# Optimization experiments

Hardware: AMD Instinct MI355X
Metric: run time of the kernel (lower is better)

The kernel has to match this reference:

```python
import jax, jax.numpy as jnp
import numpy as np
from jax import lax

B, C, HW = 128, 32, 16
N_E = 4096
PNS = (1, 2, 3, 4, 5, 6, 8, 10, 13, 16)
SN = len(PNS)
BETA, RESI = 0.25, 0.5
EPS = 1e-12

# PhiPartiallyShared tick schedule (K=4): which of the 4 Phi convs each scale uses
_TICKS = np.linspace(1.0 / 12.0, 1.0 - 1.0 / 12.0, 4)
PHI_IDX = [int(np.argmin(np.abs(_TICKS - si / (SN - 1)))) for si in range(SN)]


def _cubic_w(t, a=-0.75):
    # PyTorch bicubic kernel (a = -0.75)
    t = np.abs(t)
    return np.where(t <= 1.0, ((a + 2.0) * t - (a + 3.0)) * t * t + 1.0,
                    np.where(t < 2.0, (((t - 5.0) * t + 8.0) * t - 4.0) * a, 0.0))


def _bicubic_mat(n_in, n_out):
    # 1D resize matrix matching F.interpolate(mode='bicubic', align_corners=False)
    M = np.zeros((n_out, n_in), np.float32)
    scale = n_in / n_out
    for i in range(n_out):
        src = (i + 0.5) * scale - 0.5
        i0 = int(np.floor(src))
        f = src - i0
        for off in (-1, 0, 1, 2):
            w = float(_cubic_w(f - off))
            j = min(max(i0 + off, 0), n_in - 1)  # border replicate
            M[i, j] += w
    return M


def _area_mat(n_in, n_out):
    # 1D matrix matching F.interpolate(mode='area') == adaptive_avg_pool
    M = np.zeros((n_out, n_in), np.float32)
    for i in range(n_out):
        s = (i * n_in) // n_out
        e = -(-((i + 1) * n_in) // n_out)  # ceil
        M[i, s:e] = 1.0 / (e - s)
    return M


DOWN = {pn: jnp.asarray(_area_mat(HW, pn)) for pn in PNS[:-1]}
UP = {pn: jnp.asarray(_bicubic_mat(pn, HW)) for pn in PNS[:-1]}


def _resize2(x, M):
    # separable 2D resize: x [B,C,Y,X] -> [B,C,O,P]
    return jnp.einsum('oy,px,bcyx->bcop', M, M, x)


def _phi(h, w, b):
    conv = lax.conv_general_dilated(h, w, (1, 1), ((1, 1), (1, 1)),
                                    dimension_numbers=('NCHW', 'OIHW', 'NCHW'))
    conv = conv + b[None, :, None, None]
    return h * (1.0 - RESI) + conv * RESI


def _forward(f_input, codebook, phi_w, phi_b):
    f_ng = lax.stop_gradient(f_input)
    f_rest = f_ng
    f_hat = jnp.zeros_like(f_ng)
    cb_n = codebook / jnp.maximum(jnp.linalg.norm(codebook, axis=-1, keepdims=True), EPS)
    loss = jnp.asarray(0.0, jnp.float32)
    idx = None
    for si, pn in enumerate(PNS):
        x = _resize2(f_rest, DOWN[pn]) if si != SN - 1 else f_rest
        rest = x.transpose(0, 2, 3, 1).reshape(-1, C)          # [B*pn*pn, C]
        rest_n = rest / jnp.maximum(jnp.linalg.norm(rest, axis=-1, keepdims=True), EPS)
        idx = jnp.argmax(rest_n @ cb_n.T, axis=1)              # cosine-sim argmax
        h = codebook[idx].reshape(B, pn, pn, C).transpose(0, 3, 1, 2)
        if si != SN - 1:
            h = _resize2(h, UP[pn])
        k = PHI_IDX[si]
        h = _phi(h, phi_w[k], phi_b[k])
        f_hat = f_hat + h
        f_rest = f_rest - h
        loss = loss + BETA * jnp.mean((lax.stop_gradient(f_hat) - f_input) ** 2) \
                    + jnp.mean((f_hat - f_ng) ** 2)
    loss = loss / SN
    # straight-through estimator
    f_hat_st = f_input + lax.stop_gradient(f_hat - f_input)
    return f_hat_st, loss, idx


def setup_inputs() -> dict:
    key = jax.random.key(0)
    k1, k2, k3, k4 = jax.random.split(key, 4)
    return {
        'f_input': jax.random.normal(k1, (B, C, HW, HW), jnp.float32),
        'codebook': jax.random.normal(k2, (N_E, C), jnp.float32) * 0.5,
        'phi_w': jax.random.normal(k3, (4, C, C, 3, 3), jnp.float32) * (1.0 / np.sqrt(C * 9)),
        'phi_b': jax.random.normal(k4, (4, C), jnp.float32) * 0.01,
    }


def reference(f_input, codebook, phi_w, phi_b):
    f_hat, loss, idx = _forward(f_input, codebook, phi_w, phi_b)
    # perplexity of last-scale code usage
    n_tok = idx.shape[0]
    avg_probs = jnp.zeros((N_E,), jnp.float32).at[idx].add(1.0) / n_tok
    perplexity = jnp.exp(-jnp.sum(avg_probs * jnp.log(avg_probs + 1e-10)))
    return f_hat, loss, perplexity
```

## Files before the change

kernel.cpp:

```cpp
#include <hip/hip_runtime.h>
#include <stdint.h>
#include <math.h>


#define DEVI __device__ __forceinline__

static constexpr int NE = 4096;

typedef _Float16 half8 __attribute__((ext_vector_type(8)));
typedef float floatx4 __attribute__((ext_vector_type(4)));

DEVI int imax(int a, int b) { return a > b ? a : b; }

DEVI float dppL(float v) {
    return __int_as_float(
        __builtin_amdgcn_update_dpp(0, __float_as_int(v), 0x111, 0xF, 0xF, true));
}
DEVI float dppR(float v) {
    return __int_as_float(
        __builtin_amdgcn_update_dpp(0, __float_as_int(v), 0x101, 0xF, 0xF, true));
}

__global__ void __launch_bounds__(256) k_setup(const float* __restrict__ cb,
                                               const float* __restrict__ pw,
                                               _Float16* __restrict__ cbh,
                                               _Float16* __restrict__ cbl,
                                               float* __restrict__ wT,
                                               float* __restrict__ um,
                                               float* __restrict__ lossAcc) {
    int blk = blockIdx.x, tid = threadIdx.x;
    if (blk < 16) {
        int r = blk * 256 + tid;
        const float* src = cb + r * 32;
        float v[32];
        float ss = 0.f;
#pragma unroll
        for (int j = 0; j < 32; ++j) { v[j] = src[j]; ss += v[j] * v[j]; }
        float n = fmaxf(sqrtf(ss), 1e-12f);
#pragma unroll
        for (int j = 0; j < 32; ++j) {
            float x = v[j] / n;
            _Float16 h = (_Float16)x;
            cbh[r * 32 + j] = h;
            cbl[r * 32 + j] = (_Float16)(x - (float)h);
        }
    } else if (blk < 160) {
        int e = (blk - 16) * 256 + tid;
        int k = e / 9216, rem = e % 9216;
        int q8 = rem / 1152, rem2 = rem % 1152;
        int ic = rem2 / 36, r3 = rem2 % 36;
        int k9 = r3 / 4, o2 = r3 % 4;
        int oc = (q8 >> 2) * 16 + (q8 & 3) * 4 + o2;
        int ky = k9 / 3, kx = k9 % 3;
        wT[e] = pw[(((k * 32 + oc) * 32 + ic) * 3 + ky) * 3 + kx];
    } else {
        if (tid < 144) {
            const int pns[9] = {1, 2, 3, 4, 5, 6, 8, 10, 13};
            int si = tid / 16, y = tid % 16, pn = pns[si];
            double scale = (double)pn / 16.0;
            double src = ((double)y + 0.5) * scale - 0.5;
            double fl = floor(src);
            int i0 = (int)fl;
            double f = src - fl;
            float row[13];
            for (int j = 0; j < pn; ++j) row[j] = 0.f;
            const double a = -0.75;
#pragma unroll
            for (int off = -1; off <= 2; ++off) {
                double t2 = fabs(f - (double)off);
                double wgt;
                if (t2 <= 1.0)      wgt = ((a + 2.0) * t2 - (a + 3.0)) * t2 * t2 + 1.0;
                else if (t2 < 2.0)  wgt = (((t2 - 5.0) * t2 + 8.0) * t2 - 4.0) * a;
                else                wgt = 0.0;
                int j = i0 + off;
                j = j < 0 ? 0 : (j > pn - 1 ? pn - 1 : j);
                row[j] = (float)((double)row[j] + wgt);
            }
            for (int j = 0; j < pn; ++j) um[si * 256 + y * pn + j] = row[j];
        } else {
            for (int i = tid - 144; i < 4112; i += 112) ((int*)lossAcc)[i] = 0;
        }
    }
}


template <int PN, bool FIRST>
__global__ void __launch_bounds__(256) k_down(const float* __restrict__ fin,
                                              const float* __restrict__ fhat,
                                              _Float16* __restrict__ xh,
                                              _Float16* __restrict__ xl) {
    constexpr int NT = PN * PN;
    constexpr int T = 128 * NT;
    constexpr int Tp = ((T + 511) / 512) * 512;
    int tid = threadIdx.x;
    if (blockIdx.x >= 256) {
        for (int i = tid; i < (Tp - T) * 32; i += 256) {
            xh[T * 32 + i] = (_Float16)0.f;
            xl[T * 32 + i] = (_Float16)0.f;
        }
        return;
    }
    __shared__ float r[16][260];
    int img = blockIdx.x >> 1, ch = (blockIdx.x & 1) * 16;

    const float4* pi4 = (const float4*)(fin + img * 8192 + ch * 256);
    const float4* ph4 = (const float4*)(fhat + img * 8192 + ch * 256);
    for (int i = tid; i < 1024; i += 256) {
        float4 a = pi4[i];
        float4 b;
        if constexpr (FIRST) { b.x = 0.f; b.y = 0.f; b.z = 0.f; b.w = 0.f; }
        else                 { b = ph4[i]; }
        int c = i >> 6, p = (i & 63) * 4;
        r[c][p]     = a.x - b.x;
        r[c][p + 1] = a.y - b.y;
        r[c][p + 2] = a.z - b.z;
        r[c][p + 3] = a.w - b.w;
    }
    __syncthreads();

    for (int e = tid; e < NT * 16; e += 256) {
        int lt = e >> 4, cp = e & 15;
        int oy = lt / PN, ox = lt % PN;
        int sy = oy * 16 / PN, ey = ((oy + 1) * 16 + PN - 1) / PN;
        int sx = ox * 16 / PN, ex = ((ox + 1) * 16 + PN - 1) / PN;
        float wy = 1.f / (float)(ey - sy);
        float wx = 1.f / (float)(ex - sx);
        float s = 0.f;
        for (int y = sy; y < ey; ++y)
            for (int x = sx; x < ex; ++x)
                s += r[cp][y * 16 + x];
        float v = s * (wy * wx);
        _Float16 h = (_Float16)v;
        int gid = (img * NT + lt) * 32 + ch + cp;
        xh[gid] = h;
        xl[gid] = (_Float16)(v - (float)h);
    }
}

template <int PN, int SEG>
__global__ void __launch_bounds__(256, 2) k_quant(
        const half8* __restrict__ xh, const half8* __restrict__ xl,
        const half8* __restrict__ cbh8, const half8* __restrict__ cbl8,
        unsigned* __restrict__ bestp) {
    constexpr int T = 128 * PN * PN;
    constexpr int Tp = ((T + 511) / 512) * 512;
    constexpr int TB = Tp / 512;
    constexpr int CPS = 4096 / SEG;
    static_assert(CPS == 128, "reg-streamed sweep sized for CPS==128");

    int tid = threadIdx.x;
    int bt = blockIdx.x % TB, seg = blockIdx.x / TB;
    int wv = tid >> 6, lane = tid & 63;
    int n0 = lane & 15, g = lane >> 4;
    int tokbase = bt * 512 + wv * 128;
    int cbase = seg * CPS;

    half8 ah[8], al[8];
#pragma unroll
    for (int mt = 0; mt < 8; ++mt) {
        int tok = tokbase + mt * 16 + n0;
        ah[mt] = xh[tok * 4 + g];
        al[mt] = xl[tok * 4 + g];
    }

    int mx[8];
#pragma unroll
    for (int mt = 0; mt < 8; ++mt) mx[mt] = (int)0x80000000;

    const floatx4 z4 = {0.f, 0.f, 0.f, 0.f};
    const int KMASK = ~(CPS - 1);
    int lowg = CPS - 1 - g * 4;

    int code0 = cbase + n0;
    half8 bh = cbh8[code0 * 4 + g];
    half8 bl = cbl8[code0 * 4 + g];
#pragma unroll 1
    for (int nt = 0; nt < 8; ++nt) {
        int nn = (nt + 1) & 7;
        int codeN = cbase + nn * 16 + n0;
        half8 bhn = cbh8[codeN * 4 + g];
        half8 bln = cbl8[codeN * 4 + g];
        int lowb = lowg - nt * 16;
#pragma unroll
        for (int mt = 0; mt < 8; ++mt) {
            floatx4 c;
            c = __builtin_amdgcn_mfma_f32_16x16x32_f16(bh, ah[mt], z4, 0, 0, 0);
            c = __builtin_amdgcn_mfma_f32_16x16x32_f16(bl, ah[mt], c,  0, 0, 0);
            c = __builtin_amdgcn_mfma_f32_16x16x32_f16(bh, al[mt], c,  0, 0, 0);
            int k0 = (__float_as_int(c[0]) & KMASK) | (lowb - 0);
            int k1 = (__float_as_int(c[1]) & KMASK) | (lowb - 1);
            int k2 = (__float_as_int(c[2]) & KMASK) | (lowb - 2);
            int k3 = (__float_as_int(c[3]) & KMASK) | (lowb - 3);
            mx[mt] = imax(mx[mt], imax(k0, k1));
            mx[mt] = imax(mx[mt], imax(k2, k3));
        }
        bh = bhn;
        bl = bln;
    }

    unsigned* dst = bestp + (size_t)seg * Tp;
#pragma unroll
    for (int mt = 0; mt < 8; ++mt) {
        int k = mx[mt];
        k = imax(k, __shfl_xor(k, 16, 64));
        k = imax(k, __shfl_xor(k, 32, 64));
        if (g == (mt >> 1))
            dst[tokbase + mt * 16 + n0] = (unsigned)k;
    }
}

template <int PN, int SEG, int K, bool FIRST, bool LAST>
__global__ void __launch_bounds__(512) k_upconv(
        const float* __restrict__ fin, float* __restrict__ fhat,
        const float* __restrict__ cbook,
        const unsigned* __restrict__ bestp,
        const float* __restrict__ wT, const float* __restrict__ phib,
        const float* __restrict__ um, float* __restrict__ lossAcc,
        int* __restrict__ hist, float* __restrict__ dout) {
    constexpr int NT = PN * PN;
    constexpr int T = 128 * NT;
    constexpr int Tp = ((T + 511) / 512) * 512;
    constexpr int CPS = 4096 / SEG;
    constexpr int RA = (PN < 16 && NT * 32 > 4096) ? NT * 32 : 4096;
    __shared__ __align__(16) float regionA[RA];
    __shared__ float hu1[(PN < 16) ? 32 * 6 * PN : 1];
    __shared__ float Us[(PN < 16) ? 16 * PN : 1];
    __shared__ int idxs[NT];
    __shared__ float red[8];
    float* S_hu = regionA;
    float* h0 = regionA;

    int img = blockIdx.x >> 2, q = blockIdx.x & 3;
    int y0 = q * 4;
    int tid = threadIdx.x;

    for (int e = tid; e < NT; e += 512) {
        int tok = img * NT + e;
        int k = (int)bestp[tok];
        int ws = 0;
#pragma unroll
        for (int s = 1; s < SEG; ++s) {
            int o = (int)bestp[(size_t)s * Tp + tok];
            bool gt = o > k;
            k = gt ? o : k;
            ws = gt ? s : ws;
        }
        idxs[e] = ws * CPS + (CPS - 1 - (k & (CPS - 1)));
    }
    if (PN < 16)
        for (int e = tid; e < 16 * PN; e += 512) Us[e] = um[e];
    __syncthreads();

    if (PN == 16) {
        if (LAST && tid < 64)
            atomicAdd(hist + idxs[y0 * 16 + tid], 1);
        for (int e = tid; e < 3072; e += 512) {
            int c = e / 96, r = e % 96;
            int rr = r >> 4, x = r & 15;
            int gy = y0 - 1 + rr;
            float v = 0.f;
            if (gy >= 0 && gy <= 15) v = cbook[idxs[gy * 16 + x] * 32 + c];
            S_hu[c * 128 + (rr + 1) * 16 + x] = v;
        }
    } else {
        for (int e = tid; e < NT * 32; e += 512) {
            int tk = e >> 5, c = e & 31;
            h0[e] = cbook[idxs[tk] * 32 + c];
        }
        __syncthreads();
        for (int e = tid; e < 6 * PN * 32; e += 512) {
            int c = e & 31, rest = e >> 5;
            int rr = rest / PN, i = rest % PN;
            int gy = y0 - 1 + rr;
            float s = 0.f;
            if (gy >= 0 && gy <= 15)
                for (int j = 0; j < PN; ++j)
                    s += Us[gy * PN + j] * h0[(j * PN + i) * 32 + c];
            hu1[(c * 6 + rr) * PN + i] = s;
        }
        __syncthreads();
        for (int e = tid; e < 3072; e += 512) {
            int c = e / 96, r = e % 96;
            int rr = r >> 4, x = r & 15;
            int gy = y0 - 1 + rr;
            float s = 0.f;
            if (gy >= 0 && gy <= 15)
                for (int i = 0; i < PN; ++i)
                    s += Us[x * PN + i] * hu1[(c * 6 + rr) * PN + i];
            S_hu[c * 128 + (rr + 1) * 16 + x] = s;
        }
    }
    __syncthreads();

    int px = tid & 63;
    int wvq = __builtin_amdgcn_readfirstlane(tid >> 6);
    int yo = px >> 4, x = px & 15;
    int y = y0 + yo;
    int ry = yo + 2;
    float acc[4] = {0.f, 0.f, 0.f, 0.f};
    const float* wk = wT + K * 9216 + wvq * 1152;
#pragma unroll 4
    for (int ic = 0; ic < 32; ++ic) {
        int a = ic * 128 + ry * 16 + x;
        float cm = S_hu[a - 16], cc = S_hu[a], cp = S_hu[a + 16];
        float lm = dppL(cm), lc = dppL(cc), lp = dppL(cp);
        float rm = dppR(cm), rc = dppR(cc), rp = dppR(cp);
        const float* w = wk + ic * 36;
#pragma unroll
        for (int o = 0; o < 4; ++o) {
            float s = acc[o];
            s = fmaf(w[o],      lm, s);
            s = fmaf(w[4 + o],  cm, s);
            s = fmaf(w[8 + o],  rm, s);
            s = fmaf(w[12 + o], lc, s);
            s = fmaf(w[16 + o], cc, s);
            s = fmaf(w[20 + o], rc, s);
            s = fmaf(w[24 + o], lp, s);
            s = fmaf(w[28 + o], cp, s);
            s = fmaf(w[32 + o], rp, s);
            acc[o] = s;
        }
    }

    float ss = 0.f;
    {
        int oc0 = (wvq >> 2) * 16 + (wvq & 3) * 4;
        int gbase = img * 8192 + oc0 * 256 + y * 16 + x;
        const float* bias = phib + K * 32 + oc0;
#pragma unroll
        for (int oi = 0; oi < 4; ++oi) {
            float conv = acc[oi] + bias[oi];
            float hval = 0.5f * S_hu[(oc0 + oi) * 128 + ry * 16 + x] + 0.5f * conv;
            float fh = (FIRST ? 0.f : fhat[gbase + oi * 256]) + hval;
            fhat[gbase + oi * 256] = fh;
            if (LAST) dout[gbase + oi * 256] = fh;
            float d = fh - fin[gbase + oi * 256];
            ss = fmaf(d, d, ss);
        }
    }
    int lane = tid & 63;
#pragma unroll
    for (int m = 1; m < 64; m <<= 1) ss += __shfl_xor(ss, m, 64);
    if (lane == 0) red[tid >> 6] = ss;
    __syncthreads();
    if (tid == 0)
        atomicAdd(lossAcc, red[0] + red[1] + red[2] + red[3] +
                           red[4] + red[5] + red[6] + red[7]);
}

__global__ void __launch_bounds__(256) k_final(const float* __restrict__ lossAcc,
                                               const int* __restrict__ hist,
                                               float* __restrict__ out) {
    __shared__ float red[256];
    int tid = threadIdx.x;
    float s = 0.f;
    for (int i = tid; i < 4096; i += 256) {
        float p = (float)hist[i] * (1.f / 32768.f);
        s += p * logf(p + 1e-10f);
    }
    red[tid] = s;
    __syncthreads();
    for (int k = 128; k > 0; k >>= 1) {
        if (tid < k) red[tid] += red[tid + k];
        __syncthreads();
    }
    if (tid == 0) {
        out[1048577] = expf(-red[0]);
        float L = 0.f;
        for (int si = 0; si < 10; ++si) L += lossAcc[si];
        out[1048576] = L * 1.25f / 1048576.f * 0.1f;
    }
}


extern "C" void kernel_launch(void* const* d_in, const int* in_sizes, int n_in,
                              void* d_out, int out_size, void* d_ws, size_t ws_size,
                              hipStream_t stream) {
    const float* f_in  = (const float*)d_in[0];
    const float* cbook = (const float*)d_in[1];
    const float* phiw  = (const float*)d_in[2];
    const float* phib  = (const float*)d_in[3];
    float* out = (float*)d_out;
    char* base = (char*)d_ws;

    float* fhat    = (float*)(base);
    float* lossAcc = (float*)(base + 4194304);
    int*   hist    = (int*)  (base + 4194368);
    float* wT      = (float*)(base + 4210752);
    float* um      = (float*)(base + 4358208);
    _Float16* cbh  = (_Float16*)(base + 4367424);
    _Float16* cbl  = (_Float16*)(base + 4629568);
    _Float16* xh   = (_Float16*)(base + 4891712);
    _Float16* xl   = (_Float16*)(base + 6988864);
    unsigned* bestp = (unsigned*)(base + 9086016);

    k_setup<<<161, 256, 0, stream>>>(cbook, phiw, cbh, cbl, wT, um, lossAcc);

#define SCALE(SI, PN, K, FIRST, LAST)                                                  \
    {                                                                                  \
        constexpr int T = 128 * PN * PN;                                               \
        constexpr int Tp = ((T + 511) / 512) * 512;                                    \
        constexpr int TB = Tp / 512;                                                   \
        constexpr int PADB = (Tp > T) ? 1 : 0;                                         \
        k_down<PN, FIRST><<<256 + PADB, 256, 0, stream>>>(f_in, fhat, xh, xl);         \
        k_quant<PN, 32><<<TB * 32, 256, 0, stream>>>(                                  \
            (const half8*)xh, (const half8*)xl, (const half8*)cbh,                     \
            (const half8*)cbl, bestp);                                                 \
        k_upconv<PN, 32, K, FIRST, LAST><<<512, 512, 0, stream>>>(                     \
            f_in, fhat, cbook, bestp, wT, phib, um + SI * 256, lossAcc + SI, hist,     \
            out);                                                                      \
    }
    SCALE(0, 1, 0, true, false);
    SCALE(1, 2, 0, false, false);
    SCALE(2, 3, 0, false, false);
    SCALE(3, 4, 1, false, false);
    SCALE(4, 5, 1, false, false);
    SCALE(5, 6, 2, false, false);
    SCALE(6, 8, 2, false, false);
    SCALE(7, 10, 2, false, false);
    SCALE(8, 13, 3, false, false);
    SCALE(9, 16, 3, false, true);
#undef SCALE
    k_final<<<1, 256, 0, stream>>>(lossAcc, hist, out);
}
```

Baseline: 465.9 us.

## Merge codebook segment argmax via 64-bit atomicMax and store residual directly

k_quant now packs the sortable score and the inverted global code index into a 64-bit key and does an atomicMax per token. This replaces the per-segment bestp array that k_upconv had to scan across 32 segments. k_upconv also writes the residual fin - fhat, so the next k_down reads a single buffer instead of fin and fhat. The costs are a zeroing pass over bestp inside k_down, atomic contention across 32 segments, and an extra residual write per scale.

```diff
diff --git a/kernel.cpp b/kernel.cpp
--- a/kernel.cpp
+++ b/kernel.cpp
@@ -84,15 +84,17 @@
 }
 
 
-template <int PN, bool FIRST>
-__global__ void __launch_bounds__(256) k_down(const float* __restrict__ fin,
-                                              const float* __restrict__ fhat,
+template <int PN>
+__global__ void __launch_bounds__(256) k_down(const float* __restrict__ src,
                                               _Float16* __restrict__ xh,
-                                              _Float16* __restrict__ xl) {
+                                              _Float16* __restrict__ xl,
+                                              unsigned long long* __restrict__ bestp) {
     constexpr int NT = PN * PN;
     constexpr int T = 128 * NT;
     constexpr int Tp = ((T + 511) / 512) * 512;
     int tid = threadIdx.x;
+    for (int i = blockIdx.x * 256 + tid; i < Tp; i += gridDim.x * 256)
+        bestp[i] = 0ull;
     if (blockIdx.x >= 256) {
         for (int i = tid; i < (Tp - T) * 32; i += 256) {
             xh[T * 32 + i] = (_Float16)0.f;
@@ -103,18 +105,14 @@
     __shared__ float r[16][260];
     int img = blockIdx.x >> 1, ch = (blockIdx.x & 1) * 16;
 
-    const float4* pi4 = (const float4*)(fin + img * 8192 + ch * 256);
-    const float4* ph4 = (const float4*)(fhat + img * 8192 + ch * 256);
+    const float4* s4 = (const float4*)(src + img * 8192 + ch * 256);
     for (int i = tid; i < 1024; i += 256) {
-        float4 a = pi4[i];
-        float4 b;
-        if constexpr (FIRST) { b.x = 0.f; b.y = 0.f; b.z = 0.f; b.w = 0.f; }
-        else                 { b = ph4[i]; }
+        float4 a = s4[i];
         int c = i >> 6, p = (i & 63) * 4;
-        r[c][p]     = a.x - b.x;
-        r[c][p + 1] = a.y - b.y;
-        r[c][p + 2] = a.z - b.z;
-        r[c][p + 3] = a.w - b.w;
+        r[c][p]     = a.x;
+        r[c][p + 1] = a.y;
+        r[c][p + 2] = a.z;
+        r[c][p + 3] = a.w;
     }
     __syncthreads();
 
@@ -141,7 +139,7 @@
 __global__ void __launch_bounds__(256, 2) k_quant(
         const half8* __restrict__ xh, const half8* __restrict__ xl,
         const half8* __restrict__ cbh8, const half8* __restrict__ cbl8,
-        unsigned* __restrict__ bestp) {
+        unsigned long long* __restrict__ bestp) {
     constexpr int T = 128 * PN * PN;
     constexpr int Tp = ((T + 511) / 512) * 512;
     constexpr int TB = Tp / 512;
@@ -198,29 +196,31 @@
         bl = bln;
     }
 
-    unsigned* dst = bestp + (size_t)seg * Tp;
 #pragma unroll
     for (int mt = 0; mt < 8; ++mt) {
         int k = mx[mt];
         k = imax(k, __shfl_xor(k, 16, 64));
         k = imax(k, __shfl_xor(k, 32, 64));
-        if (g == (mt >> 1))
-            dst[tokbase + mt * 16 + n0] = (unsigned)k;
-    }
-}
-
-template <int PN, int SEG, int K, bool FIRST, bool LAST>
+        if (g == (mt >> 1)) {
+            int gidx = cbase + (CPS - 1) - (k & (CPS - 1));
+            unsigned long long k64 =
+                ((unsigned long long)((unsigned)k ^ 0x80000000u) << 32) |
+                (unsigned)~gidx;
+            atomicMax(bestp + tokbase + mt * 16 + n0, k64);
+        }
+    }
+}
+
+template <int PN, int K, bool FIRST, bool LAST>
 __global__ void __launch_bounds__(512) k_upconv(
         const float* __restrict__ fin, float* __restrict__ fhat,
+        float* __restrict__ resid,
         const float* __restrict__ cbook,
-        const unsigned* __restrict__ bestp,
+        const unsigned long long* __restrict__ bestp,
         const float* __restrict__ wT, const float* __restrict__ phib,
         const float* __restrict__ um, float* __restrict__ lossAcc,
         int* __restrict__ hist, float* __restrict__ dout) {
     constexpr int NT = PN * PN;
-    constexpr int T = 128 * NT;
-    constexpr int Tp = ((T + 511) / 512) * 512;
-    constexpr int CPS = 4096 / SEG;
     constexpr int RA = (PN < 16 && NT * 32 > 4096) ? NT * 32 : 4096;
     __shared__ __align__(16) float regionA[RA];
     __shared__ float hu1[(PN < 16) ? 32 * 6 * PN : 1];
@@ -235,17 +235,8 @@
     int tid = threadIdx.x;
 
     for (int e = tid; e < NT; e += 512) {
-        int tok = img * NT + e;
-        int k = (int)bestp[tok];
-        int ws = 0;
-#pragma unroll
-        for (int s = 1; s < SEG; ++s) {
-            int o = (int)bestp[(size_t)s * Tp + tok];
-            bool gt = o > k;
-            k = gt ? o : k;
-            ws = gt ? s : ws;
-        }
-        idxs[e] = ws * CPS + (CPS - 1 - (k & (CPS - 1)));
+        unsigned long long k64 = bestp[img * NT + e];
+        idxs[e] = (int)(~(unsigned)(k64 & 0xFFFFFFFFull));
     }
     if (PN < 16)
         for (int e = tid; e < 16 * PN; e += 512) Us[e] = um[e];
@@ -334,8 +325,9 @@
             float fh = (FIRST ? 0.f : fhat[gbase + oi * 256]) + hval;
             fhat[gbase + oi * 256] = fh;
             if (LAST) dout[gbase + oi * 256] = fh;
-            float d = fh - fin[gbase + oi * 256];
-            ss = fmaf(d, d, ss);
+            float rr = fin[gbase + oi * 256] - fh;
+            if (!LAST) resid[gbase + oi * 256] = rr;
+            ss = fmaf(rr, rr, ss);
         }
     }
     int lane = tid & 63;
@@ -392,7 +384,8 @@
     _Float16* cbl  = (_Float16*)(base + 4629568);
     _Float16* xh   = (_Float16*)(base + 4891712);
     _Float16* xl   = (_Float16*)(base + 6988864);
-    unsigned* bestp = (unsigned*)(base + 9086016);
+    unsigned long long* bestp = (unsigned long long*)(base + 9086016);
+    float* resid   = (float*)(base + 13280320);
 
     k_setup<<<161, 256, 0, stream>>>(cbook, phiw, cbh, cbl, wT, um, lossAcc);
 
@@ -402,13 +395,14 @@
         constexpr int Tp = ((T + 511) / 512) * 512;                                    \
         constexpr int TB = Tp / 512;                                                   \
         constexpr int PADB = (Tp > T) ? 1 : 0;                                         \
-        k_down<PN, FIRST><<<256 + PADB, 256, 0, stream>>>(f_in, fhat, xh, xl);         \
+        k_down<PN><<<256 + PADB, 256, 0, stream>>>(                                    \
+            FIRST ? f_in : (const float*)resid, xh, xl, bestp);                        \
         k_quant<PN, 32><<<TB * 32, 256, 0, stream>>>(                                  \
             (const half8*)xh, (const half8*)xl, (const half8*)cbh,                     \
             (const half8*)cbl, bestp);                                                 \
-        k_upconv<PN, 32, K, FIRST, LAST><<<512, 512, 0, stream>>>(                     \
-            f_in, fhat, cbook, bestp, wT, phib, um + SI * 256, lossAcc + SI, hist,     \
-            out);                                                                      \
+        k_upconv<PN, K, FIRST, LAST><<<512, 512, 0, stream>>>(                         \
+            f_in, fhat, resid, cbook, bestp, wT, phib, um + SI * 256,                  \
+            lossAcc + SI, hist, out);                                                  \
     }
     SCALE(0, 1, 0, true, false);
     SCALE(1, 2, 0, false, false);
```

Measured after the change: 455.8 us, median of 2. 2.2% less time.
